# Kernel optimization log

Hardware: AMD Instinct MI355X
Metric: run time of the kernel (lower is better)

The kernel has to match this reference:

```python
import jax, jax.numpy as jnp
import numpy as np

NO, NR, E, D = 50000, 2000, 600000, 128
NEG_SLOPE = 0.2


def setup_inputs() -> dict:
    key = jax.random.key(0)
    ks = jax.random.split(key, 16)
    p = lambda k, shape: jax.random.normal(k, shape, dtype=jnp.float32) * 0.05
    return {
        "x_order": jax.random.normal(ks[0], (NO, D), dtype=jnp.float32),
        "x_rider": jax.random.normal(ks[1], (NR, D), dtype=jnp.float32),
        "order_idx": jax.random.randint(ks[2], (E,), 0, NO),
        "rider_idx": jax.random.randint(ks[3], (E,), 0, NR),
        # GATConv layer 1 (order_input_dim=128 -> hidden_dim=128, heads=1)
        "Ws1": p(ks[4], (D, D)), "Wd1": p(ks[5], (D, D)),
        "as1": p(ks[6], (D,)), "ad1": p(ks[7], (D,)), "b1": jnp.zeros((D,), jnp.float32),
        # GATConv layer 2 (hidden_dim=128 -> output_dim=128, heads=1)
        "Ws2": p(ks[8], (D, D)), "Wd2": p(ks[9], (D, D)),
        "as2": p(ks[10], (D,)), "ad2": p(ks[11], (D,)), "b2": jnp.zeros((D,), jnp.float32),
    }


def _segment_softmax(e, seg, num_segments):
    # numerically-stable softmax over edges grouped by destination node
    m = jax.ops.segment_max(e, seg, num_segments=num_segments)
    ex = jnp.exp(e - m[seg])
    s = jax.ops.segment_sum(ex, seg, num_segments=num_segments)
    return ex / (s[seg] + 1e-16)


def _gat_bipartite(x_src, x_dst, oi, ri, Ws, Wd, a_src, a_dst, b, n_dst):
    # PyG GATConv, heads=1, bipartite (src=order, dst=rider), no self-loops
    hs = x_src @ Ws            # [NO, D]
    hd = x_dst @ Wd            # [NR, D]
    alpha_s = hs @ a_src       # [NO]
    alpha_d = hd @ a_dst       # [NR]
    e = jax.nn.leaky_relu(alpha_s[oi] + alpha_d[ri], NEG_SLOPE)  # [E]
    alpha = _segment_softmax(e, ri, n_dst)                        # [E]
    out = jax.ops.segment_sum(alpha[:, None] * hs[oi], ri, num_segments=n_dst)
    return out + b


def reference(x_order, x_rider, order_idx, rider_idx,
              Ws1, Wd1, as1, ad1, b1, Ws2, Wd2, as2, ad2, b2):
    n_rider = x_rider.shape[0]
    # layer 1: update riders; order features pass through
    r1 = jax.nn.relu(_gat_bipartite(x_order, x_rider, order_idx, rider_idx,
                                    Ws1, Wd1, as1, ad1, b1, n_rider))
    o1 = jax.nn.relu(x_order)
    # layer 2
    r2 = _gat_bipartite(o1, r1, order_idx, rider_idx,
                        Ws2, Wd2, as2, ad2, b2, n_rider)
    # per-edge gather-dot-sigmoid scoring
    scores = jnp.sum(o1[order_idx] * r2[rider_idx], axis=1)
    return jax.nn.sigmoid(scores)
```

## Files before the change

### kernel.cpp

```cpp
#include <hip/hip_runtime.h>
#include <hip/hip_fp16.h>
#include <math.h>

#define NO 50000
#define NR 2000
#define NE 600000
#define D  128
#define NEG_SLOPE 0.2f
#define CAP 448
#define SLOT 512
#define NB 256
#define CH ((NE + NB - 1) / NB)

__global__ void prep_hist(const int* __restrict__ ri, int* __restrict__ blockHist,
                          const float* __restrict__ Ws1, const float* __restrict__ as1,
                          const float* __restrict__ Wd1, const float* __restrict__ ad1,
                          const float* __restrict__ Ws2, const float* __restrict__ as2,
                          const float* __restrict__ Wd2, const float* __restrict__ ad2,
                          float* __restrict__ wsv1, float* __restrict__ wdv1,
                          float* __restrict__ wsv2, float* __restrict__ wdv2) {
    __shared__ int h[NR];
    int t = threadIdx.x;
    if (blockIdx.x < NB) {
        int b = blockIdx.x;
        for (int i = t; i < NR; i += 256) h[i] = 0;
        __syncthreads();
        int lo = b * CH;
        int hi = lo + CH; if (hi > NE) hi = NE;
        for (int i = lo + t; i < hi; i += 256) atomicAdd(&h[ri[i]], 1);
        __syncthreads();
        for (int i = t; i < NR; i += 256) blockHist[(size_t)b * NR + i] = h[i];
    } else if (t < 128) {
        int k = t;
        float s1 = 0.f, d1 = 0.f, s2 = 0.f, d2 = 0.f;
        for (int j = 0; j < D; ++j) {
            s1 += Ws1[k * D + j] * as1[j];
            d1 += Wd1[k * D + j] * ad1[j];
            s2 += Ws2[k * D + j] * as2[j];
            d2 += Wd2[k * D + j] * ad2[j];
        }
        wsv1[k] = s1; wdv1[k] = d1; wsv2[k] = s2; wdv2[k] = d2;
    }
}

__global__ void prep_scan(const float* __restrict__ x, const float* __restrict__ xr,
                          const float* __restrict__ wsv1, const float* __restrict__ wsv2,
                          const float* __restrict__ wdv1,
                          float* __restrict__ as1o, float* __restrict__ as2o,
                          float* __restrict__ ad1r, __half* __restrict__ x16,
                          int* __restrict__ blockHist, int* __restrict__ total) {
    int lane = threadIdx.x & 63;
    int b = blockIdx.x;
    if (b < NO / 4) {
        int row = b * 4 + (threadIdx.x >> 6);
        float2 xv = ((const float2*)(x + (size_t)row * D))[lane];
        float2 w1 = ((const float2*)wsv1)[lane];
        float2 w2 = ((const float2*)wsv2)[lane];
        float rx0 = fmaxf(xv.x, 0.f), rx1 = fmaxf(xv.y, 0.f);
        ((__half2*)(x16 + (size_t)row * D))[lane] = __floats2half2_rn(xv.x, xv.y);
        float a1 = xv.x * w1.x + xv.y * w1.y;
        float a2 = rx0 * w2.x + rx1 * w2.y;
        for (int off = 32; off; off >>= 1) {
            a1 += __shfl_down(a1, off);
            a2 += __shfl_down(a2, off);
        }
        if (lane == 0) { as1o[row] = a1; as2o[row] = a2; }
    } else if (b < NO / 4 + NR / 4) {
        int row = (b - NO / 4) * 4 + (threadIdx.x >> 6);
        float2 xv = ((const float2*)(xr + (size_t)row * D))[lane];
        float2 w1 = ((const float2*)wdv1)[lane];
        float a = xv.x * w1.x + xv.y * w1.y;
        for (int off = 32; off; off >>= 1) a += __shfl_down(a, off);
        if (lane == 0) ad1r[row] = a;
    } else {
        int v = b - (NO / 4 + NR / 4);
        int r = v * 4 + (threadIdx.x >> 6);
        if (r >= NR) return;
        int b0 = lane * 4;
        int v0 = blockHist[(size_t)(b0 + 0) * NR + r];
        int v1 = blockHist[(size_t)(b0 + 1) * NR + r];
        int v2 = blockHist[(size_t)(b0 + 2) * NR + r];
        int v3 = blockHist[(size_t)(b0 + 3) * NR + r];
        int s = v0 + v1 + v2 + v3;
        int incl = s;
        for (int off = 1; off < 64; off <<= 1) {
            int u = __shfl_up(incl, off);
            if (lane >= off) incl += u;
        }
        int base = incl - s;
        blockHist[(size_t)(b0 + 0) * NR + r] = base;
        blockHist[(size_t)(b0 + 1) * NR + r] = base + v0;
        blockHist[(size_t)(b0 + 2) * NR + r] = base + v0 + v1;
        blockHist[(size_t)(b0 + 3) * NR + r] = base + v0 + v1 + v2;
        int tot = __shfl(incl, 63);
        if (lane == 0) total[r] = tot;
    }
}

__global__ void scatter_kernel(const int* __restrict__ oi, const int* __restrict__ ri,
                               const int* __restrict__ blockHist,
                               int* __restrict__ sOrd) {
    __shared__ int h[NR];
    int b = blockIdx.x, t = threadIdx.x;
    for (int i = t; i < NR; i += 256) h[i] = 0;
    __syncthreads();
    int lo = b * CH;
    int hi = lo + CH; if (hi > NE) hi = NE;
    for (int i = lo + t; i < hi; i += 256) {
        int r = ri[i];
        int rank = atomicAdd(&h[r], 1);
        int pos = r * SLOT + blockHist[(size_t)b * NR + r] + rank;
        sOrd[pos] = oi[i];
    }
}

__global__ void __launch_bounds__(256)
agg12(const __half* __restrict__ x16,
      const float* __restrict__ as1o, const float* __restrict__ as2o,
      const float* __restrict__ ad1r,
      const int* __restrict__ cnt, const int* __restrict__ sOrd,
      const float* __restrict__ W1, const float* __restrict__ b1,
      const float* __restrict__ wdv2,
      const float* __restrict__ W2, const float* __restrict__ b2,
      __half* __restrict__ r216) {
    __shared__ float eL[CAP];
    __shared__ int   sO[CAP];
    __shared__ float red[256];
    __shared__ float red8[256][9];
    __shared__ float tl[D];
    int r = blockIdx.x, t = threadIdx.x;
    int base = r * SLOT, n = cnt[r];
    int grp = t >> 4, lh = t & 15;

    float ad1 = ad1r[r];
    float ls = 0.f;
    for (int i = t; i < n; i += 256) {
        int o = sOrd[base + i];
        float e = as1o[o] + ad1;
        e = (e > 0.f) ? e : NEG_SLOPE * e;
        float ex = __expf(e);
        if (i < CAP) { eL[i] = ex; sO[i] = o; }
        ls += ex;
    }
    red[t] = ls;
    __syncthreads();
    for (int off = 128; off; off >>= 1) {
        if (t < off) red[t] += red[t + off];
        __syncthreads();
    }
    float inv1 = 1.f / (red[0] + 1e-16f);
    __syncthreads();

    {
        float acc[8];
#pragma unroll
        for (int k = 0; k < 8; ++k) acc[k] = 0.f;
        if (n <= CAP) {
            int i = grp;
            for (; i + 16 < n; i += 32) {
                float a0 = eL[i], a1 = eL[i + 16];
                uint4 h0 = ((const uint4*)(x16 + (size_t)sO[i]      * D))[lh];
                uint4 h1 = ((const uint4*)(x16 + (size_t)sO[i + 16] * D))[lh];
                const __half2* p0 = (const __half2*)&h0;
                const __half2* p1 = (const __half2*)&h1;
#pragma unroll
                for (int q = 0; q < 4; ++q) {
                    float2 f0 = __half22float2(p0[q]);
                    float2 f1 = __half22float2(p1[q]);
                    acc[2 * q]     += a0 * f0.x + a1 * f1.x;
                    acc[2 * q + 1] += a0 * f0.y + a1 * f1.y;
                }
            }
            if (i < n) {
                float a0 = eL[i];
                uint4 h0 = ((const uint4*)(x16 + (size_t)sO[i] * D))[lh];
                const __half2* p0 = (const __half2*)&h0;
#pragma unroll
                for (int q = 0; q < 4; ++q) {
                    float2 f0 = __half22float2(p0[q]);
                    acc[2 * q]     += a0 * f0.x;
                    acc[2 * q + 1] += a0 * f0.y;
                }
            }
        } else {
            for (int i = grp; i < n; i += 16) {
                float a0; int o;
                if (i < CAP) { a0 = eL[i]; o = sO[i]; }
                else {
                    o = sOrd[base + i];
                    float e = as1o[o] + ad1;
                    e = (e > 0.f) ? e : NEG_SLOPE * e;
                    a0 = __expf(e);
                }
                uint4 h0 = ((const uint4*)(x16 + (size_t)o * D))[lh];
                const __half2* p0 = (const __half2*)&h0;
#pragma unroll
                for (int q = 0; q < 4; ++q) {
                    float2 f0 = __half22float2(p0[q]);
                    acc[2 * q]     += a0 * f0.x;
                    acc[2 * q + 1] += a0 * f0.y;
                }
            }
        }
#pragma unroll
        for (int k = 0; k < 8; ++k) red8[t][k] = acc[k];
    }
    __syncthreads();
    if (t < D) {
        int lh2 = t >> 3, k = t & 7;
        float s = 0.f;
        for (int g = 0; g < 16; ++g) s += red8[g * 16 + lh2][k];
        tl[t] = s * inv1;
    }
    __syncthreads();

    {
        int d = t & 127, h = t >> 7;
        float a = 0.f;
        for (int k = h * 64; k < h * 64 + 64; ++k) a += tl[k] * W1[k * D + d];
        red[t] = a;
        __syncthreads();
        if (t < 128) red[t] = fmaxf(red[t] + red[t + 128] + b1[t], 0.f) * wdv2[t];
        __syncthreads();
        for (int off = 64; off; off >>= 1) {
            if (t < off) red[t] += red[t + off];
            __syncthreads();
        }
    }
    float ad2 = red[0];
    __syncthreads();

    float ls2 = 0.f;
    for (int i = t; i < n; i += 256) {
        int o = (i < CAP) ? sO[i] : sOrd[base + i];
        float e = as2o[o] + ad2;
        e = (e > 0.f) ? e : NEG_SLOPE * e;
        float ex = __expf(e);
        if (i < CAP) eL[i] = ex;
        ls2 += ex;
    }
    red[t] = ls2;
    __syncthreads();
    for (int off = 128; off; off >>= 1) {
        if (t < off) red[t] += red[t + off];
        __syncthreads();
    }
    float inv2 = 1.f / (red[0] + 1e-16f);
    __syncthreads();

    {
        float acc[8];
#pragma unroll
        for (int k = 0; k < 8; ++k) acc[k] = 0.f;
        if (n <= CAP) {
            int i = grp;
            for (; i + 16 < n; i += 32) {
                float a0 = eL[i], a1 = eL[i + 16];
                uint4 h0 = ((const uint4*)(x16 + (size_t)sO[i]      * D))[lh];
                uint4 h1 = ((const uint4*)(x16 + (size_t)sO[i + 16] * D))[lh];
                const __half2* p0 = (const __half2*)&h0;
                const __half2* p1 = (const __half2*)&h1;
#pragma unroll
                for (int q = 0; q < 4; ++q) {
                    float2 f0 = __half22float2(p0[q]);
                    float2 f1 = __half22float2(p1[q]);
                    acc[2 * q]     += a0 * fmaxf(f0.x, 0.f) + a1 * fmaxf(f1.x, 0.f);
                    acc[2 * q + 1] += a0 * fmaxf(f0.y, 0.f) + a1 * fmaxf(f1.y, 0.f);
                }
            }
            if (i < n) {
                float a0 = eL[i];
                uint4 h0 = ((const uint4*)(x16 + (size_t)sO[i] * D))[lh];
                const __half2* p0 = (const __half2*)&h0;
#pragma unroll
                for (int q = 0; q < 4; ++q) {
                    float2 f0 = __half22float2(p0[q]);
                    acc[2 * q]     += a0 * fmaxf(f0.x, 0.f);
                    acc[2 * q + 1] += a0 * fmaxf(f0.y, 0.f);
                }
            }
        } else {
            for (int i = grp; i < n; i += 16) {
                float a0; int o;
                if (i < CAP) { a0 = eL[i]; o = sO[i]; }
                else {
                    o = sOrd[base + i];
                    float e = as2o[o] + ad2;
                    e = (e > 0.f) ? e : NEG_SLOPE * e;
                    a0 = __expf(e);
                }
                uint4 h0 = ((const uint4*)(x16 + (size_t)o * D))[lh];
                const __half2* p0 = (const __half2*)&h0;
#pragma unroll
                for (int q = 0; q < 4; ++q) {
                    float2 f0 = __half22float2(p0[q]);
                    acc[2 * q]     += a0 * fmaxf(f0.x, 0.f);
                    acc[2 * q + 1] += a0 * fmaxf(f0.y, 0.f);
                }
            }
        }
#pragma unroll
        for (int k = 0; k < 8; ++k) red8[t][k] = acc[k];
    }
    __syncthreads();
    if (t < D) {
        int lh2 = t >> 3, k = t & 7;
        float s = 0.f;
        for (int g = 0; g < 16; ++g) s += red8[g * 16 + lh2][k];
        tl[t] = s * inv2;
    }
    __syncthreads();

    {
        int d = t & 127, h = t >> 7;
        float a = 0.f;
        for (int k = h * 64; k < h * 64 + 64; ++k) a += tl[k] * W2[k * D + d];
        red[t] = a;
        __syncthreads();
        if (t < 128) r216[(size_t)r * D + t] = __float2half(red[t] + red[t + 128] + b2[t]);
    }
}

__global__ void score_edges(const __half* __restrict__ x16, const __half* __restrict__ r216,
                            const int* __restrict__ oi, const int* __restrict__ ri,
                            float* __restrict__ out) {
    int gid = blockIdx.x * blockDim.x + threadIdx.x;
    int e  = gid >> 4;
    int lh = gid & 15;
    if (e >= NE) return;
    int o = oi[e], r = ri[e];
    uint4 hx = ((const uint4*)(x16  + (size_t)o * D))[lh];
    uint4 hr = ((const uint4*)(r216 + (size_t)r * D))[lh];
    float2 a0 = __half22float2(*(const __half2*)&hx.x);
    float2 a1 = __half22float2(*(const __half2*)&hx.y);
    float2 a2 = __half22float2(*(const __half2*)&hx.z);
    float2 a3 = __half22float2(*(const __half2*)&hx.w);
    float2 b0 = __half22float2(*(const __half2*)&hr.x);
    float2 b1 = __half22float2(*(const __half2*)&hr.y);
    float2 b2 = __half22float2(*(const __half2*)&hr.z);
    float2 b3 = __half22float2(*(const __half2*)&hr.w);
    float p = fmaxf(a0.x, 0.f) * b0.x + fmaxf(a0.y, 0.f) * b0.y +
              fmaxf(a1.x, 0.f) * b1.x + fmaxf(a1.y, 0.f) * b1.y +
              fmaxf(a2.x, 0.f) * b2.x + fmaxf(a2.y, 0.f) * b2.y +
              fmaxf(a3.x, 0.f) * b3.x + fmaxf(a3.y, 0.f) * b3.y;
    p += __shfl_xor(p, 8);
    p += __shfl_xor(p, 4);
    p += __shfl_xor(p, 2);
    p += __shfl_xor(p, 1);
    if (lh == 0) out[e] = 1.f / (1.f + __expf(-p));
}

extern "C" void kernel_launch(void* const* d_in, const int* in_sizes, int n_in,
                              void* d_out, int out_size, void* d_ws, size_t ws_size,
                              hipStream_t stream) {
    const float* x_order = (const float*)d_in[0];
    const float* x_rider = (const float*)d_in[1];
    const int*   oi      = (const int*)d_in[2];
    const int*   ri      = (const int*)d_in[3];
    const float* Ws1 = (const float*)d_in[4];
    const float* Wd1 = (const float*)d_in[5];
    const float* as1 = (const float*)d_in[6];
    const float* ad1 = (const float*)d_in[7];
    const float* b1  = (const float*)d_in[8];
    const float* Ws2 = (const float*)d_in[9];
    const float* Wd2 = (const float*)d_in[10];
    const float* as2 = (const float*)d_in[11];
    const float* ad2 = (const float*)d_in[12];
    const float* b2  = (const float*)d_in[13];
    float* out = (float*)d_out;

    char* w = (char*)d_ws;
    float* wsv1 = (float*)w; w += 512;
    float* wdv1 = (float*)w; w += 512;
    float* wsv2 = (float*)w; w += 512;
    float* wdv2 = (float*)w; w += 512;
    float* as1o = (float*)w; w += (size_t)NO * 4;
    float* as2o = (float*)w; w += (size_t)NO * 4;
    float* ad1r = (float*)w; w += (size_t)NR * 4;
    int* total  = (int*)w;   w += (size_t)NR * 4;
    int* blockHist = (int*)w; w += (size_t)NB * NR * 4;
    int* sOrd   = (int*)w;   w += (size_t)NR * SLOT * 4;
    __half* x16  = (__half*)w; w += (size_t)NO * D * 2;
    __half* r216 = (__half*)w; w += (size_t)NR * D * 2;

    prep_hist<<<NB + 1, 256, 0, stream>>>(ri, blockHist,
                                          Ws1, as1, Wd1, ad1, Ws2, as2, Wd2, ad2,
                                          wsv1, wdv1, wsv2, wdv2);
    prep_scan<<<NO / 4 + NR / 4 + 500, 256, 0, stream>>>(x_order, x_rider,
                                                         wsv1, wsv2, wdv1,
                                                         as1o, as2o, ad1r, x16,
                                                         blockHist, total);
    scatter_kernel<<<NB, 256, 0, stream>>>(oi, ri, blockHist, sOrd);
    agg12<<<NR, 256, 0, stream>>>(x16, as1o, as2o, ad1r, total, sOrd,
                                  Ws1, b1, wdv2, Ws2, b2, r216);
    score_edges<<<(NE * 16 + 255) / 256, 256, 0, stream>>>(x16, r216, oi, ri, out);
}
```

Measured before the change: 218.6 us.

## Fuse edge scoring into per-rider aggregation kernel and merge softmax passes

The separate score_edges kernel is removed. The aggregation kernel now stores the original edge id next to each order index and scores every edge of its rider right after computing r2, so r2 stays in registers and the fp16 r2 round-trip through global memory goes away. The exp-sum passes are merged into the weighted aggregation loops and the tree reductions become wavefront shuffles, which cuts barriers and repeated gathers. In exchange there is a third gather pass per block, output writes become scattered, and the scatter step now writes int2 entries.

```diff
diff --git a/kernel.cpp b/kernel.cpp
--- a/kernel.cpp
+++ b/kernel.cpp
@@ -99,7 +99,7 @@
 
 __global__ void scatter_kernel(const int* __restrict__ oi, const int* __restrict__ ri,
                                const int* __restrict__ blockHist,
-                               int* __restrict__ sOrd) {
+                               int2* __restrict__ sOE) {
     __shared__ int h[NR];
     int b = blockIdx.x, t = threadIdx.x;
     for (int i = t; i < NR; i += 256) h[i] = 0;
@@ -110,7 +110,7 @@
         int r = ri[i];
         int rank = atomicAdd(&h[r], 1);
         int pos = r * SLOT + blockHist[(size_t)b * NR + r] + rank;
-        sOrd[pos] = oi[i];
+        sOE[pos] = make_int2(oi[i], i);
     }
 }
 
@@ -118,90 +118,97 @@
 agg12(const __half* __restrict__ x16,
       const float* __restrict__ as1o, const float* __restrict__ as2o,
       const float* __restrict__ ad1r,
-      const int* __restrict__ cnt, const int* __restrict__ sOrd,
+      const int* __restrict__ cnt, const int2* __restrict__ sOE,
       const float* __restrict__ W1, const float* __restrict__ b1,
       const float* __restrict__ wdv2,
       const float* __restrict__ W2, const float* __restrict__ b2,
-      __half* __restrict__ r216) {
-    __shared__ float eL[CAP];
+      float* __restrict__ out) {
     __shared__ int   sO[CAP];
+    __shared__ int   sE[CAP];
     __shared__ float red[256];
     __shared__ float red8[256][9];
     __shared__ float tl[D];
+    __shared__ float r2s[D];
+    __shared__ float wred[4];
     int r = blockIdx.x, t = threadIdx.x;
     int base = r * SLOT, n = cnt[r];
     int grp = t >> 4, lh = t & 15;
 
+    int lim = n < CAP ? n : CAP;
+    for (int i = t; i < lim; i += 256) {
+        int2 v = sOE[base + i];
+        sO[i] = v.x; sE[i] = v.y;
+    }
     float ad1 = ad1r[r];
+    __syncthreads();
+
+    float acc[8];
+#pragma unroll
+    for (int k = 0; k < 8; ++k) acc[k] = 0.f;
     float ls = 0.f;
-    for (int i = t; i < n; i += 256) {
-        int o = sOrd[base + i];
-        float e = as1o[o] + ad1;
-        e = (e > 0.f) ? e : NEG_SLOPE * e;
-        float ex = __expf(e);
-        if (i < CAP) { eL[i] = ex; sO[i] = o; }
-        ls += ex;
-    }
-    red[t] = ls;
-    __syncthreads();
-    for (int off = 128; off; off >>= 1) {
-        if (t < off) red[t] += red[t + off];
-        __syncthreads();
-    }
-    float inv1 = 1.f / (red[0] + 1e-16f);
-    __syncthreads();
-
+    if (n <= CAP) {
+        int i = grp;
+        for (; i + 16 < n; i += 32) {
+            int o0 = sO[i], o1 = sO[i + 16];
+            uint4 h0 = ((const uint4*)(x16 + (size_t)o0 * D))[lh];
+            uint4 h1 = ((const uint4*)(x16 + (size_t)o1 * D))[lh];
+            float e0 = as1o[o0] + ad1;
+            float e1 = as1o[o1] + ad1;
+            e0 = (e0 > 0.f) ? e0 : NEG_SLOPE * e0;
+            e1 = (e1 > 0.f) ? e1 : NEG_SLOPE * e1;
+            float a0 = __expf(e0), a1 = __expf(e1);
+            ls += a0 + a1;
+            const __half2* p0 = (const __half2*)&h0;
+            const __half2* p1 = (const __half2*)&h1;
+#pragma unroll
+            for (int q = 0; q < 4; ++q) {
+                float2 f0 = __half22float2(p0[q]);
+                float2 f1 = __half22float2(p1[q]);
+                acc[2 * q]     += a0 * f0.x + a1 * f1.x;
+                acc[2 * q + 1] += a0 * f0.y + a1 * f1.y;
+            }
+        }
+        if (i < n) {
+            int o0 = sO[i];
+            uint4 h0 = ((const uint4*)(x16 + (size_t)o0 * D))[lh];
+            float e0 = as1o[o0] + ad1;
+            e0 = (e0 > 0.f) ? e0 : NEG_SLOPE * e0;
+            float a0 = __expf(e0);
+            ls += a0;
+            const __half2* p0 = (const __half2*)&h0;
+#pragma unroll
+            for (int q = 0; q < 4; ++q) {
+                float2 f0 = __half22float2(p0[q]);
+                acc[2 * q]     += a0 * f0.x;
+                acc[2 * q + 1] += a0 * f0.y;
+            }
+        }
+    } else {
+        for (int i = grp; i < n; i += 16) {
+            int o0 = (i < CAP) ? sO[i] : sOE[base + i].x;
+            uint4 h0 = ((const uint4*)(x16 + (size_t)o0 * D))[lh];
+            float e0 = as1o[o0] + ad1;
+            e0 = (e0 > 0.f) ? e0 : NEG_SLOPE * e0;
+            float a0 = __expf(e0);
+            ls += a0;
+            const __half2* p0 = (const __half2*)&h0;
+#pragma unroll
+            for (int q = 0; q < 4; ++q) {
+                float2 f0 = __half22float2(p0[q]);
+                acc[2 * q]     += a0 * f0.x;
+                acc[2 * q + 1] += a0 * f0.y;
+            }
+        }
+    }
     {
-        float acc[8];
-#pragma unroll
-        for (int k = 0; k < 8; ++k) acc[k] = 0.f;
-        if (n <= CAP) {
-            int i = grp;
-            for (; i + 16 < n; i += 32) {
-                float a0 = eL[i], a1 = eL[i + 16];
-                uint4 h0 = ((const uint4*)(x16 + (size_t)sO[i]      * D))[lh];
-                uint4 h1 = ((const uint4*)(x16 + (size_t)sO[i + 16] * D))[lh];
-                const __half2* p0 = (const __half2*)&h0;
-                const __half2* p1 = (const __half2*)&h1;
-#pragma unroll
-                for (int q = 0; q < 4; ++q) {
-                    float2 f0 = __half22float2(p0[q]);
-                    float2 f1 = __half22float2(p1[q]);
-                    acc[2 * q]     += a0 * f0.x + a1 * f1.x;
-                    acc[2 * q + 1] += a0 * f0.y + a1 * f1.y;
-                }
-            }
-            if (i < n) {
-                float a0 = eL[i];
-                uint4 h0 = ((const uint4*)(x16 + (size_t)sO[i] * D))[lh];
-                const __half2* p0 = (const __half2*)&h0;
-#pragma unroll
-                for (int q = 0; q < 4; ++q) {
-                    float2 f0 = __half22float2(p0[q]);
-                    acc[2 * q]     += a0 * f0.x;
-                    acc[2 * q + 1] += a0 * f0.y;
-                }
-            }
-        } else {
-            for (int i = grp; i < n; i += 16) {
-                float a0; int o;
-                if (i < CAP) { a0 = eL[i]; o = sO[i]; }
-                else {
-                    o = sOrd[base + i];
-                    float e = as1o[o] + ad1;
-                    e = (e > 0.f) ? e : NEG_SLOPE * e;
-                    a0 = __expf(e);
-                }
-                uint4 h0 = ((const uint4*)(x16 + (size_t)o * D))[lh];
-                const __half2* p0 = (const __half2*)&h0;
-#pragma unroll
-                for (int q = 0; q < 4; ++q) {
-                    float2 f0 = __half22float2(p0[q]);
-                    acc[2 * q]     += a0 * f0.x;
-                    acc[2 * q + 1] += a0 * f0.y;
-                }
-            }
-        }
+        float lsv = (lh == 0) ? ls : 0.f;
+        lsv += __shfl_down(lsv, 32);
+        lsv += __shfl_down(lsv, 16);
+        lsv += __shfl_down(lsv, 8);
+        lsv += __shfl_down(lsv, 4);
+        lsv += __shfl_down(lsv, 2);
+        lsv += __shfl_down(lsv, 1);
+        if ((t & 63) == 0) wred[t >> 6] = lsv;
 #pragma unroll
         for (int k = 0; k < 8; ++k) red8[t][k] = acc[k];
     }
@@ -209,7 +216,9 @@
     if (t < D) {
         int lh2 = t >> 3, k = t & 7;
         float s = 0.f;
+#pragma unroll
         for (int g = 0; g < 16; ++g) s += red8[g * 16 + lh2][k];
+        float inv1 = 1.f / (wred[0] + wred[1] + wred[2] + wred[3] + 1e-16f);
         tl[t] = s * inv1;
     }
     __syncthreads();
@@ -219,86 +228,89 @@
         float a = 0.f;
         for (int k = h * 64; k < h * 64 + 64; ++k) a += tl[k] * W1[k * D + d];
         red[t] = a;
-        __syncthreads();
-        if (t < 128) red[t] = fmaxf(red[t] + red[t + 128] + b1[t], 0.f) * wdv2[t];
-        __syncthreads();
-        for (int off = 64; off; off >>= 1) {
-            if (t < off) red[t] += red[t + off];
-            __syncthreads();
-        }
-    }
-    float ad2 = red[0];
-    __syncthreads();
-
-    float ls2 = 0.f;
-    for (int i = t; i < n; i += 256) {
-        int o = (i < CAP) ? sO[i] : sOrd[base + i];
-        float e = as2o[o] + ad2;
-        e = (e > 0.f) ? e : NEG_SLOPE * e;
-        float ex = __expf(e);
-        if (i < CAP) eL[i] = ex;
-        ls2 += ex;
-    }
-    red[t] = ls2;
-    __syncthreads();
-    for (int off = 128; off; off >>= 1) {
-        if (t < off) red[t] += red[t + off];
-        __syncthreads();
-    }
-    float inv2 = 1.f / (red[0] + 1e-16f);
-    __syncthreads();
-
+    }
+    __syncthreads();
     {
-        float acc[8];
-#pragma unroll
-        for (int k = 0; k < 8; ++k) acc[k] = 0.f;
-        if (n <= CAP) {
-            int i = grp;
-            for (; i + 16 < n; i += 32) {
-                float a0 = eL[i], a1 = eL[i + 16];
-                uint4 h0 = ((const uint4*)(x16 + (size_t)sO[i]      * D))[lh];
-                uint4 h1 = ((const uint4*)(x16 + (size_t)sO[i + 16] * D))[lh];
-                const __half2* p0 = (const __half2*)&h0;
-                const __half2* p1 = (const __half2*)&h1;
-#pragma unroll
-                for (int q = 0; q < 4; ++q) {
-                    float2 f0 = __half22float2(p0[q]);
-                    float2 f1 = __half22float2(p1[q]);
-                    acc[2 * q]     += a0 * fmaxf(f0.x, 0.f) + a1 * fmaxf(f1.x, 0.f);
-                    acc[2 * q + 1] += a0 * fmaxf(f0.y, 0.f) + a1 * fmaxf(f1.y, 0.f);
-                }
-            }
-            if (i < n) {
-                float a0 = eL[i];
-                uint4 h0 = ((const uint4*)(x16 + (size_t)sO[i] * D))[lh];
-                const __half2* p0 = (const __half2*)&h0;
-#pragma unroll
-                for (int q = 0; q < 4; ++q) {
-                    float2 f0 = __half22float2(p0[q]);
-                    acc[2 * q]     += a0 * fmaxf(f0.x, 0.f);
-                    acc[2 * q + 1] += a0 * fmaxf(f0.y, 0.f);
-                }
-            }
-        } else {
-            for (int i = grp; i < n; i += 16) {
-                float a0; int o;
-                if (i < CAP) { a0 = eL[i]; o = sO[i]; }
-                else {
-                    o = sOrd[base + i];
-                    float e = as2o[o] + ad2;
-                    e = (e > 0.f) ? e : NEG_SLOPE * e;
-                    a0 = __expf(e);
-                }
-                uint4 h0 = ((const uint4*)(x16 + (size_t)o * D))[lh];
-                const __half2* p0 = (const __half2*)&h0;
-#pragma unroll
-                for (int q = 0; q < 4; ++q) {
-                    float2 f0 = __half22float2(p0[q]);
-                    acc[2 * q]     += a0 * fmaxf(f0.x, 0.f);
-                    acc[2 * q + 1] += a0 * fmaxf(f0.y, 0.f);
-                }
-            }
-        }
+        float v = 0.f;
+        if (t < 128) v = fmaxf(red[t] + red[t + 128] + b1[t], 0.f) * wdv2[t];
+        v += __shfl_down(v, 32);
+        v += __shfl_down(v, 16);
+        v += __shfl_down(v, 8);
+        v += __shfl_down(v, 4);
+        v += __shfl_down(v, 2);
+        v += __shfl_down(v, 1);
+        if ((t & 63) == 0) wred[t >> 6] = v;
+    }
+    __syncthreads();
+    float ad2 = wred[0] + wred[1] + wred[2] + wred[3];
+    __syncthreads();
+
+#pragma unroll
+    for (int k = 0; k < 8; ++k) acc[k] = 0.f;
+    ls = 0.f;
+    if (n <= CAP) {
+        int i = grp;
+        for (; i + 16 < n; i += 32) {
+            int o0 = sO[i], o1 = sO[i + 16];
+            uint4 h0 = ((const uint4*)(x16 + (size_t)o0 * D))[lh];
+            uint4 h1 = ((const uint4*)(x16 + (size_t)o1 * D))[lh];
+            float e0 = as2o[o0] + ad2;
+            float e1 = as2o[o1] + ad2;
+            e0 = (e0 > 0.f) ? e0 : NEG_SLOPE * e0;
+            e1 = (e1 > 0.f) ? e1 : NEG_SLOPE * e1;
+            float a0 = __expf(e0), a1 = __expf(e1);
+            ls += a0 + a1;
+            const __half2* p0 = (const __half2*)&h0;
+            const __half2* p1 = (const __half2*)&h1;
+#pragma unroll
+            for (int q = 0; q < 4; ++q) {
+                float2 f0 = __half22float2(p0[q]);
+                float2 f1 = __half22float2(p1[q]);
+                acc[2 * q]     += a0 * fmaxf(f0.x, 0.f) + a1 * fmaxf(f1.x, 0.f);
+                acc[2 * q + 1] += a0 * fmaxf(f0.y, 0.f) + a1 * fmaxf(f1.y, 0.f);
+            }
+        }
+        if (i < n) {
+            int o0 = sO[i];
+            uint4 h0 = ((const uint4*)(x16 + (size_t)o0 * D))[lh];
+            float e0 = as2o[o0] + ad2;
+            e0 = (e0 > 0.f) ? e0 : NEG_SLOPE * e0;
+            float a0 = __expf(e0);
+            ls += a0;
+            const __half2* p0 = (const __half2*)&h0;
+#pragma unroll
+            for (int q = 0; q < 4; ++q) {
+                float2 f0 = __half22float2(p0[q]);
+                acc[2 * q]     += a0 * fmaxf(f0.x, 0.f);
+                acc[2 * q + 1] += a0 * fmaxf(f0.y, 0.f);
+            }
+        }
+    } else {
+        for (int i = grp; i < n; i += 16) {
+            int o0 = (i < CAP) ? sO[i] : sOE[base + i].x;
+            uint4 h0 = ((const uint4*)(x16 + (size_t)o0 * D))[lh];
+            float e0 = as2o[o0] + ad2;
+            e0 = (e0 > 0.f) ? e0 : NEG_SLOPE * e0;
+            float a0 = __expf(e0);
+            ls += a0;
+            const __half2* p0 = (const __half2*)&h0;
+#pragma unroll
+            for (int q = 0; q < 4; ++q) {
+                float2 f0 = __half22float2(p0[q]);
+                acc[2 * q]     += a0 * fmaxf(f0.x, 0.f);
+                acc[2 * q + 1] += a0 * fmaxf(f0.y, 0.f);
+            }
+        }
+    }
+    {
+        float lsv = (lh == 0) ? ls : 0.f;
+        lsv += __shfl_down(lsv, 32);
+        lsv += __shfl_down(lsv, 16);
+        lsv += __shfl_down(lsv, 8);
+        lsv += __shfl_down(lsv, 4);
+        lsv += __shfl_down(lsv, 2);
+        lsv += __shfl_down(lsv, 1);
+        if ((t & 63) == 0) wred[t >> 6] = lsv;
 #pragma unroll
         for (int k = 0; k < 8; ++k) red8[t][k] = acc[k];
     }
@@ -306,7 +318,9 @@
     if (t < D) {
         int lh2 = t >> 3, k = t & 7;
         float s = 0.f;
+#pragma unroll
         for (int g = 0; g < 16; ++g) s += red8[g * 16 + lh2][k];
+        float inv2 = 1.f / (wred[0] + wred[1] + wred[2] + wred[3] + 1e-16f);
         tl[t] = s * inv2;
     }
     __syncthreads();
@@ -316,38 +330,76 @@
         float a = 0.f;
         for (int k = h * 64; k < h * 64 + 64; ++k) a += tl[k] * W2[k * D + d];
         red[t] = a;
-        __syncthreads();
-        if (t < 128) r216[(size_t)r * D + t] = __float2half(red[t] + red[t + 128] + b2[t]);
-    }
-}
-
-__global__ void score_edges(const __half* __restrict__ x16, const __half* __restrict__ r216,
-                            const int* __restrict__ oi, const int* __restrict__ ri,
-                            float* __restrict__ out) {
-    int gid = blockIdx.x * blockDim.x + threadIdx.x;
-    int e  = gid >> 4;
-    int lh = gid & 15;
-    if (e >= NE) return;
-    int o = oi[e], r = ri[e];
-    uint4 hx = ((const uint4*)(x16  + (size_t)o * D))[lh];
-    uint4 hr = ((const uint4*)(r216 + (size_t)r * D))[lh];
-    float2 a0 = __half22float2(*(const __half2*)&hx.x);
-    float2 a1 = __half22float2(*(const __half2*)&hx.y);
-    float2 a2 = __half22float2(*(const __half2*)&hx.z);
-    float2 a3 = __half22float2(*(const __half2*)&hx.w);
-    float2 b0 = __half22float2(*(const __half2*)&hr.x);
-    float2 b1 = __half22float2(*(const __half2*)&hr.y);
-    float2 b2 = __half22float2(*(const __half2*)&hr.z);
-    float2 b3 = __half22float2(*(const __half2*)&hr.w);
-    float p = fmaxf(a0.x, 0.f) * b0.x + fmaxf(a0.y, 0.f) * b0.y +
-              fmaxf(a1.x, 0.f) * b1.x + fmaxf(a1.y, 0.f) * b1.y +
-              fmaxf(a2.x, 0.f) * b2.x + fmaxf(a2.y, 0.f) * b2.y +
-              fmaxf(a3.x, 0.f) * b3.x + fmaxf(a3.y, 0.f) * b3.y;
-    p += __shfl_xor(p, 8);
-    p += __shfl_xor(p, 4);
-    p += __shfl_xor(p, 2);
-    p += __shfl_xor(p, 1);
-    if (lh == 0) out[e] = 1.f / (1.f + __expf(-p));
+    }
+    __syncthreads();
+    if (t < 128) r2s[t] = red[t] + red[t + 128] + b2[t];
+    __syncthreads();
+
+    float r2v[8];
+#pragma unroll
+    for (int k = 0; k < 8; ++k) r2v[k] = r2s[lh * 8 + k];
+    if (n <= CAP) {
+        int i = grp;
+        for (; i + 16 < n; i += 32) {
+            int o0 = sO[i], o1 = sO[i + 16];
+            int e0 = sE[i], e1 = sE[i + 16];
+            uint4 h0 = ((const uint4*)(x16 + (size_t)o0 * D))[lh];
+            uint4 h1 = ((const uint4*)(x16 + (size_t)o1 * D))[lh];
+            const __half2* p0 = (const __half2*)&h0;
+            const __half2* p1 = (const __half2*)&h1;
+            float pa = 0.f, pb = 0.f;
+#pragma unroll
+            for (int q = 0; q < 4; ++q) {
+                float2 f0 = __half22float2(p0[q]);
+                float2 f1 = __half22float2(p1[q]);
+                pa += fmaxf(f0.x, 0.f) * r2v[2 * q] + fmaxf(f0.y, 0.f) * r2v[2 * q + 1];
+                pb += fmaxf(f1.x, 0.f) * r2v[2 * q] + fmaxf(f1.y, 0.f) * r2v[2 * q + 1];
+            }
+            pa += __shfl_xor(pa, 8); pb += __shfl_xor(pb, 8);
+            pa += __shfl_xor(pa, 4); pb += __shfl_xor(pb, 4);
+            pa += __shfl_xor(pa, 2); pb += __shfl_xor(pb, 2);
+            pa += __shfl_xor(pa, 1); pb += __shfl_xor(pb, 1);
+            if (lh == 0) {
+                out[e0] = 1.f / (1.f + __expf(-pa));
+                out[e1] = 1.f / (1.f + __expf(-pb));
+            }
+        }
+        if (i < n) {
+            int o0 = sO[i], e0 = sE[i];
+            uint4 h0 = ((const uint4*)(x16 + (size_t)o0 * D))[lh];
+            const __half2* p0 = (const __half2*)&h0;
+            float pa = 0.f;
+#pragma unroll
+            for (int q = 0; q < 4; ++q) {
+                float2 f0 = __half22float2(p0[q]);
+                pa += fmaxf(f0.x, 0.f) * r2v[2 * q] + fmaxf(f0.y, 0.f) * r2v[2 * q + 1];
+            }
+            pa += __shfl_xor(pa, 8);
+            pa += __shfl_xor(pa, 4);
+            pa += __shfl_xor(pa, 2);
+            pa += __shfl_xor(pa, 1);
+            if (lh == 0) out[e0] = 1.f / (1.f + __expf(-pa));
+        }
+    } else {
+        for (int i = grp; i < n; i += 16) {
+            int o0, e0;
+            if (i < CAP) { o0 = sO[i]; e0 = sE[i]; }
+            else { int2 v = sOE[base + i]; o0 = v.x; e0 = v.y; }
+            uint4 h0 = ((const uint4*)(x16 + (size_t)o0 * D))[lh];
+            const __half2* p0 = (const __half2*)&h0;
+            float pa = 0.f;
+#pragma unroll
+            for (int q = 0; q < 4; ++q) {
+                float2 f0 = __half22float2(p0[q]);
+                pa += fmaxf(f0.x, 0.f) * r2v[2 * q] + fmaxf(f0.y, 0.f) * r2v[2 * q + 1];
+            }
+            pa += __shfl_xor(pa, 8);
+            pa += __shfl_xor(pa, 4);
+            pa += __shfl_xor(pa, 2);
+            pa += __shfl_xor(pa, 1);
+            if (lh == 0) out[e0] = 1.f / (1.f + __expf(-pa));
+        }
+    }
 }
 
 extern "C" void kernel_launch(void* const* d_in, const int* in_sizes, int n_in,
@@ -379,9 +431,8 @@
     float* ad1r = (float*)w; w += (size_t)NR * 4;
     int* total  = (int*)w;   w += (size_t)NR * 4;
     int* blockHist = (int*)w; w += (size_t)NB * NR * 4;
-    int* sOrd   = (int*)w;   w += (size_t)NR * SLOT * 4;
-    __half* x16  = (__half*)w; w += (size_t)NO * D * 2;
-    __half* r216 = (__half*)w; w += (size_t)NR * D * 2;
+    int2* sOE   = (int2*)w;  w += (size_t)NR * SLOT * 8;
+    __half* x16 = (__half*)w; w += (size_t)NO * D * 2;
 
     prep_hist<<<NB + 1, 256, 0, stream>>>(ri, blockHist,
                                           Ws1, as1, Wd1, ad1, Ws2, as2, Wd2, ad2,
@@ -390,8 +441,7 @@
                                                          wsv1, wsv2, wdv1,
                                                          as1o, as2o, ad1r, x16,
                                                          blockHist, total);
-    scatter_kernel<<<NB, 256, 0, stream>>>(oi, ri, blockHist, sOrd);
-    agg12<<<NR, 256, 0, stream>>>(x16, as1o, as2o, ad1r, total, sOrd,
-                                  Ws1, b1, wdv2, Ws2, b2, r216);
-    score_edges<<<(NE * 16 + 255) / 256, 256, 0, stream>>>(x16, r216, oi, ri, out);
+    scatter_kernel<<<NB, 256, 0, stream>>>(oi, ri, blockHist, sOE);
+    agg12<<<NR, 256, 0, stream>>>(x16, as1o, as2o, ad1r, total, sOE,
+                                  Ws1, b1, wdv2, Ws2, b2, out);
 }
```

Result: no change. 214.5 us (-1.9%).
